# Kernel tuning notes

Measured on AMD Instinct MI355X. Metric: run time of the kernel, lower is better.

## Reference

```python
import jax, jax.numpy as jnp
from jax import lax
import numpy as np

B, C, H, W = 4, 256, 128, 128
NC, NH = 19, 8
HD = C // NH
SCALE = HD ** -0.5
MOM = 0.1

def conv2d(x, w, b=None, pad=0, groups=1):
    y = lax.conv_general_dilated(x, w, (1, 1), [(pad, pad), (pad, pad)],
                                 dimension_numbers=('NCHW', 'OIHW', 'NCHW'),
                                 feature_group_count=groups)
    return y if b is None else y + b[None, :, None, None]

def layernorm(x, g, b, eps=1e-5):
    # LN over channel dim (original permutes to NHWC, LN, permutes back)
    mu = x.mean(1, keepdims=True)
    var = jnp.mean((x - mu) ** 2, 1, keepdims=True)
    return (x - mu) / jnp.sqrt(var + eps) * g[None, :, None, None] + b[None, :, None, None]

def setup_inputs():
    key = jax.random.key(0)
    ks = jax.random.split(key, 24)
    s = 0.02
    mem = jax.random.normal(ks[12], (1, NC, C), jnp.float32)
    mem = mem / jnp.linalg.norm(mem, axis=2, keepdims=True)  # F.normalize(dim=2)
    return dict(
        low=jax.random.normal(ks[0], (B, C, H, W), jnp.float32),
        high=jax.random.normal(ks[1], (B, C, H, W), jnp.float32),
        g_low=jnp.ones((C,), jnp.float32), b_low=jnp.zeros((C,), jnp.float32),
        g_high=jnp.ones((C,), jnp.float32), b_high=jnp.zeros((C,), jnp.float32),
        g_mlp=jnp.ones((C,), jnp.float32), b_mlp=jnp.zeros((C,), jnp.float32),
        w_q_dw=jax.random.normal(ks[2], (C, 1, 3, 3), jnp.float32) * s, b_q_dw=jnp.zeros((C,), jnp.float32),
        w_q_pw=jax.random.normal(ks[3], (C, C, 1, 1), jnp.float32) * s, b_q_pw=jnp.zeros((C,), jnp.float32),
        w_ml1=jax.random.normal(ks[4], (C, C // 4, 1, 1), jnp.float32) * s,
        w_ml2=jax.random.normal(ks[5], (NC, C, 1, 1), jnp.float32) * s,
        w_align=jax.random.normal(ks[6], (C, C // 4, 1, 1), jnp.float32) * s,
        w_kv=jax.random.normal(ks[7], (2 * C, C), jnp.float32) * s, b_kv=jnp.zeros((2 * C,), jnp.float32),
        memory=mem,
        w_proj=jax.random.normal(ks[8], (C, C, 1, 1), jnp.float32) * s, b_proj=jnp.zeros((C,), jnp.float32),
        w_mlp1=jax.random.normal(ks[9], (4 * C, C, 1, 1), jnp.float32) * s, b_mlp1=jnp.zeros((4 * C,), jnp.float32),
        w_mlp_dw=jax.random.normal(ks[10], (4 * C, 1, 3, 3), jnp.float32) * s, b_mlp_dw=jnp.zeros((4 * C,), jnp.float32),
        w_mlp2=jax.random.normal(ks[11], (C, 4 * C, 1, 1), jnp.float32) * s, b_mlp2=jnp.zeros((C,), jnp.float32),
    )

def _cpga(low, high, g_low, b_low, g_high, b_high, g_mlp, b_mlp,
          w_q_dw, b_q_dw, w_q_pw, b_q_pw, w_ml1, w_ml2, w_align,
          w_kv, b_kv, memory, w_proj, b_proj,
          w_mlp1, b_mlp1, w_mlp_dw, b_mlp_dw, w_mlp2, b_mlp2):
    query = layernorm(low, g_low, b_low)
    kv_in = layernorm(high, g_high, b_high)
    fused = (query + kv_in) * 0.5
    # CFEmbedding: learned class mask -> spatial softmax -> class prototypes
    mask = conv2d(conv2d(fused, w_ml1, groups=4), w_ml2)           # [B,NC,H,W]
    mask = jax.nn.softmax(mask.reshape(B, NC, H * W), axis=-1)
    xa = conv2d(fused, w_align, groups=4).reshape(B, C, H * W)
    cf = jnp.einsum('bnl,bcl->bnc', mask, xa)                      # [B,NC,C]
    cf = (1.0 - MOM) * cf + MOM * memory                           # memory mix (eval mode)
    kv = jnp.einsum('bnc,dc->bnd', cf, w_kv) + b_kv                # [B,NC,2C]
    k, v = jnp.split(kv, 2, axis=-1)                               # [B,NC,C] each
    # query path: depthwise-separable 3x3 conv
    q = conv2d(query, w_q_dw, b_q_dw, pad=1, groups=C)
    q = conv2d(q, w_q_pw, b_q_pw).reshape(B, NH, HD, H * W)        # [B,NH,HD,HW]
    kh = k.reshape(B, NC, NH, HD)
    vh = v.reshape(B, NC, NH, HD)
    attn = jnp.einsum('bhdl,bnhd->bhln', q, kh) * SCALE            # [B,NH,HW,NC]
    attn = jnp.max(attn, axis=-1, keepdims=True) - attn            # custom max-subtract
    attn = jax.nn.softmax(attn, axis=-1)
    out = jnp.einsum('bhln,bnhd->bhdl', attn, vh).reshape(B, C, H, W)
    out = conv2d(out, w_proj, b_proj) + low                        # residual 1
    # conv FFN: 1x1 expand -> depthwise 3x3 -> GELU -> 1x1 project
    y = layernorm(out, g_mlp, b_mlp)
    y = conv2d(y, w_mlp1, b_mlp1)
    y = conv2d(y, w_mlp_dw, b_mlp_dw, pad=1, groups=4 * C)
    y = jax.nn.gelu(y, approximate=False)
    y = conv2d(y, w_mlp2, b_mlp2)
    return out + y                                                 # residual 2

def reference(low, high, g_low, b_low, g_high, b_high, g_mlp, b_mlp,
              w_q_dw, b_q_dw, w_q_pw, b_q_pw, w_ml1, w_ml2, w_align,
              w_kv, b_kv, memory, w_proj, b_proj,
              w_mlp1, b_mlp1, w_mlp_dw, b_mlp_dw, w_mlp2, b_mlp2):
    return _cpga(low, high, g_low, b_low, g_high, b_high, g_mlp, b_mlp,
                 w_q_dw, b_q_dw, w_q_pw, b_q_pw, w_ml1, w_ml2, w_align,
                 w_kv, b_kv, memory, w_proj, b_proj,
                 w_mlp1, b_mlp1, w_mlp_dw, b_mlp_dw, w_mlp2, b_mlp2)
```

## Files before the change

kernel.cpp:

```cpp
#include <hip/hip_runtime.h>
#include <hip/hip_bf16.h>
#include <math.h>

using bf16 = __hip_bfloat16;
typedef __attribute__((ext_vector_type(8))) short bf16x8s;
typedef __attribute__((ext_vector_type(4))) float f32x4;

#define HWD 16384
#define CD 256
#define BD 4
#define NCD 19
#define SCALE_F 0.17677669529663687f

#define O_GLOW    0
#define O_BLOW    256
#define O_GHIGH   512
#define O_BHIGH   768
#define O_GMLP    1024
#define O_BMLP    1280
#define O_WQDW    1536
#define O_BQDW    3840
#define O_WQPW    4096
#define O_BQPW    69632
#define O_WML1    69888
#define O_WML2    86272
#define O_WALIGN  91136
#define O_WKV     107520
#define O_BKV     238592
#define O_MEM     239104
#define O_WPROJ   243968
#define O_BPROJ   309504
#define O_WMLP1   309760
#define O_BMLP1   571904
#define O_WMLPDW  572928
#define O_BMLPDW  582144
#define O_WMLP2   583168
#define O_BMLP2   845312
#define WTOTAL    845568

__device__ __forceinline__ float bfv(const bf16* p){ return __bfloat162float(*p); }
__device__ __forceinline__ float ldi(const void* p, size_t i, bool f32){
  return f32 ? ((const float*)p)[i] : __bfloat162float(((const bf16*)p)[i]);
}
__device__ __forceinline__ void sto(void* p, size_t i, float v, bool f32){
  if (f32) ((float*)p)[i] = v; else ((bf16*)p)[i] = __float2bfloat16(v);
}

__device__ __forceinline__ void gld16(const bf16* g, bf16* l){
  __builtin_amdgcn_global_load_lds(
      (const __attribute__((address_space(1))) unsigned int*)g,
      (__attribute__((address_space(3))) unsigned int*)l, 16, 0, 0);
}

__global__ void detect_kernel(const unsigned* __restrict__ g, int* __restrict__ flag){
  if (threadIdx.x == 0) *flag = (g[0] == 0x3F800000u) ? 1 : 0;
}

struct WSrc { const void* p[24]; };
__global__ __launch_bounds__(256) void convert_kernel(WSrc a, bf16* __restrict__ WB,
                                                      const int* __restrict__ flag){
  const bool fin = *flag != 0;
  const int SZ[24] = {256,256,256,256,256,256, 2304,256, 65536,256,
                      16384,4864,16384, 131072,512,4864, 65536,256,
                      262144,1024, 9216,1024, 262144,256};
  size_t i = (size_t)blockIdx.x*256 + threadIdx.x;
  if (i >= WTOTAL) return;
  size_t base = 0; int seg = 0; size_t loc = 0;
  #pragma unroll
  for (int s = 0; s < 24; s++){
    if (i >= base && i < base + (size_t)SZ[s]){ seg = s; loc = i - base; }
    base += (size_t)SZ[s];
  }
  WB[i] = __float2bfloat16(ldi(a.p[seg], loc, fin));
}

__global__ __launch_bounds__(256) void ln_fuse_kernel(
    const void* __restrict__ low, const void* __restrict__ high,
    const bf16* __restrict__ WB, bf16* __restrict__ Q, bf16* __restrict__ F,
    const int* __restrict__ flag){
  const bool fin = *flag != 0;
  union SMU { float red[16][64][4]; bf16 tile[64][256]; };
  __shared__ SMU sm;
  __shared__ float stats[4][64];
  int t = threadIdx.x;
  int pq = t & 15, cs = t >> 4;
  int lg0 = blockIdx.x * 64;
  int b = lg0 >> 14, ll0 = lg0 & (HWD-1);
  size_t pbase = (size_t)b*CD*HWD + (size_t)ll0 + pq*4;
  int c0 = cs*16;

  float s1[4]={0,0,0,0}, s2[4]={0,0,0,0}, u1[4]={0,0,0,0}, u2[4]={0,0,0,0};
  for (int k=0;k<16;k++){
    size_t off = pbase + (size_t)(c0+k)*HWD;
    float xl[4], xh[4];
    if (fin){
      float4 a = *(const float4*)((const float*)low + off);
      float4 h = *(const float4*)((const float*)high + off);
      xl[0]=a.x; xl[1]=a.y; xl[2]=a.z; xl[3]=a.w;
      xh[0]=h.x; xh[1]=h.y; xh[2]=h.z; xh[3]=h.w;
    } else {
      ushort4 a = *(const ushort4*)((const bf16*)low + off);
      ushort4 h = *(const ushort4*)((const bf16*)high + off);
      const bf16* ap=(const bf16*)&a; const bf16* hp=(const bf16*)&h;
      #pragma unroll
      for (int q=0;q<4;q++){ xl[q]=__bfloat162float(ap[q]); xh[q]=__bfloat162float(hp[q]); }
    }
    #pragma unroll
    for (int q=0;q<4;q++){
      s1[q]+=xl[q]; s2[q]+=xl[q]*xl[q];
      u1[q]+=xh[q]; u2[q]+=xh[q]*xh[q];
    }
  }
  #pragma unroll
  for (int q=0;q<4;q++){
    sm.red[cs][pq*4+q][0]=s1[q]; sm.red[cs][pq*4+q][1]=s2[q];
    sm.red[cs][pq*4+q][2]=u1[q]; sm.red[cs][pq*4+q][3]=u2[q];
  }
  __syncthreads();
  if (t < 64){
    float a=0.f,b2=0.f,c=0.f,d=0.f;
    #pragma unroll
    for (int j=0;j<16;j++){
      a+=sm.red[j][t][0]; b2+=sm.red[j][t][1];
      c+=sm.red[j][t][2]; d+=sm.red[j][t][3];
    }
    float ml=a*(1.f/CD), vl=b2*(1.f/CD)-ml*ml;
    float mh=c*(1.f/CD), vh=d*(1.f/CD)-mh*mh;
    stats[0][t]=ml; stats[1][t]=rsqrtf(vl+1e-5f);
    stats[2][t]=mh; stats[3][t]=rsqrtf(vh+1e-5f);
  }
  __syncthreads();
  float mlq[4],rlq[4],mhq[4],rhq[4];
  #pragma unroll
  for (int q=0;q<4;q++){
    mlq[q]=stats[0][pq*4+q]; rlq[q]=stats[1][pq*4+q];
    mhq[q]=stats[2][pq*4+q]; rhq[q]=stats[3][pq*4+q];
  }

  for (int k=0;k<16;k++){
    int c = c0+k;
    size_t off = pbase + (size_t)c*HWD;
    float xl[4];
    if (fin){
      float4 a = *(const float4*)((const float*)low + off);
      xl[0]=a.x; xl[1]=a.y; xl[2]=a.z; xl[3]=a.w;
    } else {
      ushort4 a = *(const ushort4*)((const bf16*)low + off);
      const bf16* ap=(const bf16*)&a;
      #pragma unroll
      for (int q=0;q<4;q++) xl[q]=__bfloat162float(ap[q]);
    }
    float g = bfv(WB+O_GLOW+c), bb = bfv(WB+O_BLOW+c);
    #pragma unroll
    for (int q=0;q<4;q++)
      sm.tile[pq*4+q][c] = __float2bfloat16((xl[q]-mlq[q])*rlq[q]*g + bb);
  }
  __syncthreads();
  {
    bf16* qb = Q + (size_t)lg0*CD;
    const uint4* src = (const uint4*)&sm.tile[0][0];
    #pragma unroll
    for (int it=0; it<8; it++)
      *(uint4*)(qb + ((size_t)it*256 + t)*8) = src[it*256 + t];
  }
  __syncthreads();

  for (int k=0;k<16;k++){
    int c = c0+k;
    size_t off = pbase + (size_t)c*HWD;
    float xl[4], xh[4];
    if (fin){
      float4 a = *(const float4*)((const float*)low + off);
      float4 h = *(const float4*)((const float*)high + off);
      xl[0]=a.x; xl[1]=a.y; xl[2]=a.z; xl[3]=a.w;
      xh[0]=h.x; xh[1]=h.y; xh[2]=h.z; xh[3]=h.w;
    } else {
      ushort4 a = *(const ushort4*)((const bf16*)low + off);
      ushort4 h = *(const ushort4*)((const bf16*)high + off);
      const bf16* ap=(const bf16*)&a; const bf16* hp=(const bf16*)&h;
      #pragma unroll
      for (int q=0;q<4;q++){ xl[q]=__bfloat162float(ap[q]); xh[q]=__bfloat162float(hp[q]); }
    }
    float gl = bfv(WB+O_GLOW+c),  bl = bfv(WB+O_BLOW+c);
    float gh = bfv(WB+O_GHIGH+c), bh = bfv(WB+O_BHIGH+c);
    #pragma unroll
    for (int q=0;q<4;q++){
      float qv = (xl[q]-mlq[q])*rlq[q]*gl + bl;
      float hv = (xh[q]-mhq[q])*rhq[q]*gh + bh;
      sm.tile[pq*4+q][c] = __float2bfloat16(0.5f*(qv+hv));
    }
  }
  __syncthreads();
  {
    bf16* fb = F + (size_t)lg0*CD;
    const uint4* src = (const uint4*)&sm.tile[0][0];
    #pragma unroll
    for (int it=0; it<8; it++)
      *(uint4*)(fb + ((size_t)it*256 + t)*8) = src[it*256 + t];
  }
}

__global__ __launch_bounds__(256) void ln_kernel(
    const bf16* __restrict__ x, const bf16* __restrict__ WB, bf16* __restrict__ out){
  int lg = blockIdx.x*256 + threadIdx.x;
  const bf16* xr = x + (size_t)lg*CD;
  float s1=0.f, s2=0.f;
  for (int v8=0; v8<32; v8++){
    uint4 vv = *(const uint4*)(xr + v8*8);
    const bf16* bb = (const bf16*)&vv;
    #pragma unroll
    for (int i=0;i<8;i++){ float x0 = __bfloat162float(bb[i]); s1+=x0; s2+=x0*x0; }
  }
  float m = s1*(1.f/CD), v = s2*(1.f/CD)-m*m, r = rsqrtf(v+1e-5f);
  bf16* orr = out + (size_t)lg*CD;
  for (int v8=0; v8<32; v8++){
    uint4 vv = *(const uint4*)(xr + v8*8);
    const bf16* bb = (const bf16*)&vv;
    #pragma unroll
    for (int i=0;i<8;i++){
      int c = v8*8+i;
      orr[c] = __float2bfloat16((__bfloat162float(bb[i])-m)*r*bfv(WB+O_GMLP+c) + bfv(WB+O_BMLP+c));
    }
  }
}

template<int K, bool GROUPED, int OUTMODE, int RESMODE, bool HASBIAS, bool SWAP>
__global__ __launch_bounds__(256) void gemm_kernel(
    const bf16* __restrict__ X, int xstride,
    const bf16* __restrict__ W, const bf16* __restrict__ bias,
    const void* __restrict__ resv, void* __restrict__ outv,
    int ostride, int co_limit, int out_off, const int* __restrict__ flag){
  __shared__ bf16 As[64*32];
  __shared__ bf16 Bs[256*32];
  int t = threadIdx.x, w = t>>6, lane = t&63;
  int l0 = blockIdx.x*256;
  int co0 = blockIdx.y*64;
  int koff = GROUPED ? co0 : 0;
  f32x4 acc[4][4];
  #pragma unroll
  for (int i=0;i<4;i++)
    #pragma unroll
    for (int j=0;j<4;j++) acc[i][j] = (f32x4){0.f,0.f,0.f,0.f};

  int sub = lane>>2, kp = lane&3;
  int a_co = co0 + w*16 + sub; if (a_co >= co_limit) a_co = co_limit-1;
  const bf16* aW = W + (size_t)a_co*K + kp*8;
  const bf16* bRow = X + (size_t)(l0 + w*64 + sub)*xstride + koff + kp*8;
  bf16* aL = As + w*512;
  int frow = lane & 15, fk = (lane>>4)*8;
  const bf16* xrd = Bs + ((w*64 + frow)*32 + fk);
  const bf16* wrd = As + (frow*32 + fk);

  for (int k0 = 0; k0 < K; k0 += 32){
    __syncthreads();
    gld16(aW + k0, aL);
    #pragma unroll
    for (int j=0;j<4;j++)
      gld16(bRow + (size_t)j*16*xstride + k0, Bs + (size_t)(w*4+j)*512);
    __syncthreads();
    bf16x8s xf[4], wf[4];
    #pragma unroll
    for (int i=0;i<4;i++){
      xf[i] = *(const bf16x8s*)(xrd + i*512);
      wf[i] = *(const bf16x8s*)(wrd + i*512);
    }
    #pragma unroll
    for (int i=0;i<4;i++)
      #pragma unroll
      for (int j=0;j<4;j++)
        acc[i][j] = SWAP
          ? __builtin_amdgcn_mfma_f32_16x16x32_bf16(wf[i], xf[j], acc[i][j], 0,0,0)
          : __builtin_amdgcn_mfma_f32_16x16x32_bf16(xf[i], wf[j], acc[i][j], 0,0,0);
  }

  const bool fio = *flag != 0;
  #pragma unroll
  for (int i=0;i<4;i++){
    #pragma unroll
    for (int j=0;j<4;j++){
      #pragma unroll
      for (int r=0;r<4;r++){
        int l, co;
        if (SWAP){ co = co0 + i*16 + (lane>>4)*4 + r; l = l0 + w*64 + j*16 + (lane&15); }
        else     { l = l0 + w*64 + i*16 + (lane>>4)*4 + r; co = co0 + j*16 + (lane&15); }
        float v = acc[i][j][r];
        if (HASBIAS) v += __bfloat162float(bias[co]);
        if (RESMODE==2){
          int b = l>>14, ll = l & (HWD-1);
          v += ldi(resv, ((size_t)(b*CD+co))*HWD + ll, fio);
        }
        if (RESMODE==1) v += __bfloat162float(((const bf16*)resv)[(size_t)l*CD + co]);
        if (OUTMODE==0) ((bf16*)outv)[(size_t)l*ostride + co] = __float2bfloat16(v);
        else if (OUTMODE==1){ if (co < co_limit) ((float*)outv)[(size_t)l*ostride + co] = v; }
        else sto(outv, (size_t)out_off + (size_t)co*HWD + l, v, fio);
      }
    }
  }
}

template<int CH, bool GELU>
__global__ __launch_bounds__(256) void dw3x3_kernel(
    const bf16* __restrict__ x, const bf16* __restrict__ w,
    const bf16* __restrict__ bias, bf16* __restrict__ out){
  constexpr int CPG = CH/8;
  constexpr int PPI = 256/CPG;
  constexpr int PPB = PPI*8;
  int t = threadIdx.x;
  int cg = t % CPG, pr = t / CPG;
  int c0 = cg*8;
  float wv[8][9], bv[8];
  #pragma unroll
  for (int i=0;i<8;i++){
    bv[i] = __bfloat162float(bias[c0+i]);
    #pragma unroll
    for (int k=0;k<9;k++) wv[i][k] = __bfloat162float(w[(c0+i)*9+k]);
  }
  int p0 = blockIdx.x * PPB;
  for (int it=0; it<8; it++){
    int px = p0 + it*PPI + pr;
    int l = px & (HWD-1);
    int y = l >> 7, xx = l & 127;
    float acc[8];
    #pragma unroll
    for (int i=0;i<8;i++) acc[i] = bv[i];
    #pragma unroll
    for (int dy=-1;dy<=1;dy++){
      int yy = y+dy; if ((unsigned)yy >= 128u) continue;
      #pragma unroll
      for (int dx=-1;dx<=1;dx++){
        int x2 = xx+dx; if ((unsigned)x2 >= 128u) continue;
        const bf16* pp = x + ((size_t)px + dy*128 + dx)*CH + c0;
        uint4 vv = *(const uint4*)pp;
        const bf16* bb = (const bf16*)&vv;
        #pragma unroll
        for (int i=0;i<8;i++) acc[i] += wv[i][(dy+1)*3+dx+1]*__bfloat162float(bb[i]);
      }
    }
    bf16* orow = out + (size_t)px*CH + c0;
    #pragma unroll
    for (int i=0;i<8;i++){
      float v = acc[i];
      if (GELU) v = 0.5f*v*(1.f+erff(v*0.70710678118f));
      orow[i] = __float2bfloat16(v);
    }
  }
}

__global__ __launch_bounds__(256) void pmax_kernel(const float* __restrict__ M, float* __restrict__ PMX){
  int b = blockIdx.y, tile = blockIdx.x, t = threadIdx.x;
  float mx[NCD];
  #pragma unroll
  for (int n=0;n<NCD;n++) mx[n] = -1e30f;
  for (int p = t; p < 512; p += 256){
    const float* r = M + ((size_t)b*HWD + tile*512 + p)*NCD;
    #pragma unroll
    for (int n=0;n<NCD;n++) mx[n] = fmaxf(mx[n], r[n]);
  }
  int lane = t&63, wv = t>>6;
  __shared__ float red[4][NCD];
  #pragma unroll
  for (int n=0;n<NCD;n++){
    float v = mx[n];
    for (int o=32;o;o>>=1) v = fmaxf(v, __shfl_down(v,o));
    if (lane==0) red[wv][n] = v;
  }
  __syncthreads();
  if (t < NCD)
    PMX[(b*32+tile)*NCD + t] = fmaxf(fmaxf(red[0][t],red[1][t]), fmaxf(red[2][t],red[3][t]));
}

__global__ void fmax_kernel(const float* __restrict__ PMX, float* __restrict__ MX, float* __restrict__ DEN){
  int t = threadIdx.x;
  if (t < BD*NCD){
    int b = t / NCD, n = t % NCD;
    float v = -1e30f;
    for (int i=0;i<32;i++) v = fmaxf(v, PMX[(b*32+i)*NCD + n]);
    MX[t] = v; DEN[t] = 0.f;
  }
}

__global__ __launch_bounds__(256) void exp_kernel(float* __restrict__ M,
    const float* __restrict__ MX, float* __restrict__ DEN){
  int b = blockIdx.y, t = threadIdx.x;
  float* r = M + ((size_t)b*HWD + blockIdx.x*256 + t)*NCD;
  float den[NCD];
  #pragma unroll
  for (int n=0;n<NCD;n++){ float e = expf(r[n] - MX[b*NCD+n]); r[n] = e; den[n] = e; }
  int lane = t&63, wv = t>>6;
  __shared__ float red[4][NCD];
  #pragma unroll
  for (int n=0;n<NCD;n++){
    float v = den[n];
    for (int o=32;o;o>>=1) v += __shfl_down(v,o);
    if (lane==0) red[wv][n] = v;
  }
  __syncthreads();
  if (t < NCD) atomicAdd(&DEN[b*NCD+t], red[0][t]+red[1][t]+red[2][t]+red[3][t]);
}

__global__ __launch_bounds__(256) void cfp_kernel(const float* __restrict__ M,
    const bf16* __restrict__ xa, float* __restrict__ PCF){
  int b = blockIdx.y, lt = blockIdx.x, c = threadIdx.x;
  float acc[NCD];
  #pragma unroll
  for (int n=0;n<NCD;n++) acc[n] = 0.f;
  for (int p=0;p<256;p++){
    size_t l = (size_t)b*HWD + lt*256 + p;
    float xv = __bfloat162float(xa[l*CD + c]);
    const float* e = M + l*NCD;
    #pragma unroll
    for (int n=0;n<NCD;n++) acc[n] += e[n]*xv;
  }
  float* o = PCF + ((size_t)(b*64+lt)*NCD)*CD + c;
  #pragma unroll
  for (int n=0;n<NCD;n++) o[n*CD] = acc[n];
}

__global__ __launch_bounds__(256) void cfr_kernel(const float* __restrict__ PCF,
    const float* __restrict__ DEN, float* __restrict__ CF){
  int idx = blockIdx.x*256 + threadIdx.x;
  if (idx >= BD*NCD*CD) return;
  int c = idx & 255, bn = idx >> 8;
  int b = bn / NCD, n = bn % NCD;
  float s = 0.f;
  for (int lt=0; lt<64; lt++) s += PCF[((size_t)(b*64+lt)*NCD + n)*CD + c];
  CF[(size_t)bn*CD + c] = s / DEN[b*NCD+n];
}

__global__ __launch_bounds__(256) void kv_kernel(const float* __restrict__ CF,
    const bf16* __restrict__ WB, float* __restrict__ KV){
  int idx = blockIdx.x*256 + threadIdx.x;
  if (idx >= BD*NCD*512) return;
  int d = idx & 511, bn = idx >> 9;
  int n = bn % NCD;
  float acc = bfv(WB + O_BKV + d);
  const float* cfr = CF + (size_t)bn*CD;
  const bf16* mr = WB + O_MEM + n*CD;
  const bf16* wr = WB + O_WKV + (size_t)d*CD;
  for (int c=0;c<CD;c++)
    acc += (0.9f*cfr[c] + 0.1f*bfv(mr+c)) * bfv(wr+c);
  KV[(size_t)bn*512 + d] = acc;
}

__global__ __launch_bounds__(256) void attn_kernel(const bf16* __restrict__ q,
    const float* __restrict__ KV, bf16* __restrict__ out){
  __shared__ float ks[NCD][256], vs[NCD][256];
  int t = threadIdx.x;
  int b = blockIdx.y, lt = blockIdx.x;
  for (int i=t; i<NCD*512; i+=256){
    int n = i>>9, d = i&511;
    float v = KV[(size_t)(b*NCD+n)*512 + d];
    if (d < 256) ks[n][d] = v; else vs[n][d-256] = v;
  }
  __syncthreads();
  int p = t & 31, h = t >> 5;
  size_t lg = (size_t)b*HWD + lt*32 + p;
  const bf16* qr = q + lg*CD + h*32;
  float qd[32];
  #pragma unroll
  for (int v8=0; v8<4; v8++){
    uint4 vv = *(const uint4*)(qr + v8*8);
    const bf16* bb = (const bf16*)&vv;
    #pragma unroll
    for (int i=0;i<8;i++) qd[v8*8+i] = __bfloat162float(bb[i]);
  }
  float s[NCD];
  #pragma unroll
  for (int n=0;n<NCD;n++){
    const float* kr = &ks[n][h*32];
    float a = 0.f;
    #pragma unroll
    for (int d=0;d<32;d++) a += qd[d]*kr[d];
    s[n] = a * SCALE_F;
  }
  float mn = s[0];
  #pragma unroll
  for (int n=1;n<NCD;n++) mn = fminf(mn, s[n]);
  float sum = 0.f;
  #pragma unroll
  for (int n=0;n<NCD;n++){ s[n] = expf(mn - s[n]); sum += s[n]; }
  float inv = 1.f/sum;
  bf16* orow = out + lg*CD + h*32;
  #pragma unroll
  for (int d=0;d<32;d++){
    float o = 0.f;
    #pragma unroll
    for (int n=0;n<NCD;n++) o += s[n]*vs[n][h*32+d];
    orow[d] = __float2bfloat16(o*inv);
  }
}

extern "C" void kernel_launch(void* const* d_in, const int* in_sizes, int n_in,
                              void* d_out, int out_size, void* d_ws, size_t ws_size,
                              hipStream_t stream){
  const void* low  = d_in[0];
  const void* high = d_in[1];

  char* ws = (char*)d_ws;
  bf16* B1 = (bf16*)(ws);
  bf16* B2 = (bf16*)(ws + ((size_t)32<<20));
  bf16* B3 = (bf16*)(ws + ((size_t)64<<20));
  bf16* B4 = (bf16*)(ws + ((size_t)96<<20));
  float* M  = (float*)(ws + ((size_t)128<<20));
  float* PCF= (float*)(ws + ((size_t)134<<20));
  bf16* WB  = (bf16*)(ws + ((size_t)140<<20));
  float* PMX= (float*)(ws + ((size_t)142<<20));
  float* MX = (float*)(ws + ((size_t)142<<20) + (64<<10));
  float* DEN= (float*)(ws + ((size_t)142<<20) + (80<<10));
  float* CF = (float*)(ws + ((size_t)142<<20) + (96<<10));
  float* KV = (float*)(ws + ((size_t)142<<20) + (256<<10));
  int* FLAG = (int*)  (ws + ((size_t)142<<20) + (512<<10));

  dim3 blk(256);

  detect_kernel<<<1, 64, 0, stream>>>((const unsigned*)d_in[2], FLAG);

  WSrc src;
  for (int i=0;i<24;i++) src.p[i] = d_in[i+2];
  convert_kernel<<<(WTOTAL+255)/256, blk, 0, stream>>>(src, WB, FLAG);

  ln_fuse_kernel<<<1024, blk, 0, stream>>>(low, high, WB, B1, B2, FLAG);
  gemm_kernel<64,true,0,0,false,false><<<dim3(256,4), blk, 0, stream>>>(
      B2, 256, WB+O_WML1, nullptr, nullptr, B3, 256, 256, 0, FLAG);
  gemm_kernel<256,false,1,0,false,false><<<dim3(256,1), blk, 0, stream>>>(
      B3, 256, WB+O_WML2, nullptr, nullptr, M, NCD, NCD, 0, FLAG);
  pmax_kernel<<<dim3(32,BD), blk, 0, stream>>>(M, PMX);
  fmax_kernel<<<1, 128, 0, stream>>>(PMX, MX, DEN);
  exp_kernel<<<dim3(64,BD), blk, 0, stream>>>(M, MX, DEN);
  gemm_kernel<64,true,0,0,false,false><<<dim3(256,4), blk, 0, stream>>>(
      B2, 256, WB+O_WALIGN, nullptr, nullptr, B3, 256, 256, 0, FLAG);
  cfp_kernel<<<dim3(64,BD), blk, 0, stream>>>(M, B3, PCF);
  cfr_kernel<<<(BD*NCD*CD+255)/256, blk, 0, stream>>>(PCF, DEN, CF);
  kv_kernel<<<(BD*NCD*512+255)/256, blk, 0, stream>>>(CF, WB, KV);
  dw3x3_kernel<256,false><<<1024, blk, 0, stream>>>(B1, WB+O_WQDW, WB+O_BQDW, B2);
  gemm_kernel<256,false,0,0,true,false><<<dim3(256,4), blk, 0, stream>>>(
      B2, 256, WB+O_WQPW, WB+O_BQPW, nullptr, B3, 256, 256, 0, FLAG);
  attn_kernel<<<dim3(512,BD), blk, 0, stream>>>(B3, KV, B2);
  gemm_kernel<256,false,0,2,true,false><<<dim3(256,4), blk, 0, stream>>>(
      B2, 256, WB+O_WPROJ, WB+O_BPROJ, low, B1, 256, 256, 0, FLAG);
  ln_kernel<<<256, blk, 0, stream>>>(B1, WB, B2);
  for (int b = 0; b < BD; b++){
    gemm_kernel<256,false,0,0,true,false><<<dim3(64,16), blk, 0, stream>>>(
        B2 + (size_t)b*HWD*CD, 256, WB+O_WMLP1, WB+O_BMLP1, nullptr, B3, 1024, 1024, 0, FLAG);
    dw3x3_kernel<1024,true><<<1024, blk, 0, stream>>>(B3, WB+O_WMLPDW, WB+O_BMLPDW, B4);
    gemm_kernel<1024,false,2,1,true,true><<<dim3(64,4), blk, 0, stream>>>(
        B4, 1024, WB+O_WMLP2, WB+O_BMLP2, B1 + (size_t)b*HWD*CD, d_out, 0, 256, b*CD*HWD, FLAG);
  }
}
```

Measured before the change: 945.7 us.

## Swizzle LN shared tile, fuse global passes, add smaller L-tile GEMM variants

The LN fuse kernel now reads low/high only once in its final pass. It keeps the averaged values in registers while writing the normalized low tile to shared memory with an XOR swizzle, which avoids bank conflicts on the column-strided stores. It also gets a launch-bounds occupancy hint. The GEMM kernel gains an L-tile template parameter, so the 19-class GEMM and the K=1024 MLP2 projection run with 128-row tiles and twice as many blocks, improving occupancy on under-filled launches. The trade-offs are more register pressure from the 64-float register array and less weight reuse per block.

```diff
diff --git a/kernel.cpp b/kernel.cpp
--- a/kernel.cpp
+++ b/kernel.cpp
@@ -74,7 +74,9 @@
   WB[i] = __float2bfloat16(ldi(a.p[seg], loc, fin));
 }
 
-__global__ __launch_bounds__(256) void ln_fuse_kernel(
+#define TSWZ(row, c) ((c) ^ (((row) >> 2) << 3))
+
+__global__ __launch_bounds__(256, 4) void ln_fuse_kernel(
     const void* __restrict__ low, const void* __restrict__ high,
     const bf16* __restrict__ WB, bf16* __restrict__ Q, bf16* __restrict__ F,
     const int* __restrict__ flag){
@@ -137,34 +139,8 @@
     mhq[q]=stats[2][pq*4+q]; rhq[q]=stats[3][pq*4+q];
   }
 
-  for (int k=0;k<16;k++){
-    int c = c0+k;
-    size_t off = pbase + (size_t)c*HWD;
-    float xl[4];
-    if (fin){
-      float4 a = *(const float4*)((const float*)low + off);
-      xl[0]=a.x; xl[1]=a.y; xl[2]=a.z; xl[3]=a.w;
-    } else {
-      ushort4 a = *(const ushort4*)((const bf16*)low + off);
-      const bf16* ap=(const bf16*)&a;
-      #pragma unroll
-      for (int q=0;q<4;q++) xl[q]=__bfloat162float(ap[q]);
-    }
-    float g = bfv(WB+O_GLOW+c), bb = bfv(WB+O_BLOW+c);
-    #pragma unroll
-    for (int q=0;q<4;q++)
-      sm.tile[pq*4+q][c] = __float2bfloat16((xl[q]-mlq[q])*rlq[q]*g + bb);
-  }
-  __syncthreads();
-  {
-    bf16* qb = Q + (size_t)lg0*CD;
-    const uint4* src = (const uint4*)&sm.tile[0][0];
-    #pragma unroll
-    for (int it=0; it<8; it++)
-      *(uint4*)(qb + ((size_t)it*256 + t)*8) = src[it*256 + t];
-  }
-  __syncthreads();
-
+  float fv[16][4];
+  #pragma unroll
   for (int k=0;k<16;k++){
     int c = c0+k;
     size_t off = pbase + (size_t)c*HWD;
@@ -185,18 +161,42 @@
     float gh = bfv(WB+O_GHIGH+c), bh = bfv(WB+O_BHIGH+c);
     #pragma unroll
     for (int q=0;q<4;q++){
+      int row = pq*4+q;
       float qv = (xl[q]-mlq[q])*rlq[q]*gl + bl;
       float hv = (xh[q]-mhq[q])*rhq[q]*gh + bh;
-      sm.tile[pq*4+q][c] = __float2bfloat16(0.5f*(qv+hv));
+      sm.tile[row][TSWZ(row, c)] = __float2bfloat16(qv);
+      fv[k][q] = 0.5f*(qv+hv);
+    }
+  }
+  __syncthreads();
+  {
+    bf16* qb = Q + (size_t)lg0*CD;
+    #pragma unroll
+    for (int it=0; it<8; it++){
+      int idx = it*256 + t;
+      int row = idx >> 5, col = (idx & 31)*8;
+      *(uint4*)(qb + (size_t)idx*8) = *(const uint4*)(&sm.tile[row][TSWZ(row, col)]);
+    }
+  }
+  __syncthreads();
+  #pragma unroll
+  for (int k=0;k<16;k++){
+    int c = c0+k;
+    #pragma unroll
+    for (int q=0;q<4;q++){
+      int row = pq*4+q;
+      sm.tile[row][TSWZ(row, c)] = __float2bfloat16(fv[k][q]);
     }
   }
   __syncthreads();
   {
     bf16* fb = F + (size_t)lg0*CD;
-    const uint4* src = (const uint4*)&sm.tile[0][0];
-    #pragma unroll
-    for (int it=0; it<8; it++)
-      *(uint4*)(fb + ((size_t)it*256 + t)*8) = src[it*256 + t];
+    #pragma unroll
+    for (int it=0; it<8; it++){
+      int idx = it*256 + t;
+      int row = idx >> 5, col = (idx & 31)*8;
+      *(uint4*)(fb + (size_t)idx*8) = *(const uint4*)(&sm.tile[row][TSWZ(row, col)]);
+    }
   }
 }
 
@@ -224,16 +224,19 @@
   }
 }
 
-template<int K, bool GROUPED, int OUTMODE, int RESMODE, bool HASBIAS, bool SWAP>
+template<int LT, int K, bool GROUPED, int OUTMODE, int RESMODE, bool HASBIAS, bool SWAP>
 __global__ __launch_bounds__(256) void gemm_kernel(
     const bf16* __restrict__ X, int xstride,
     const bf16* __restrict__ W, const bf16* __restrict__ bias,
     const void* __restrict__ resv, void* __restrict__ outv,
     int ostride, int co_limit, int out_off, const int* __restrict__ flag){
+  constexpr int IF = LT/64;
+  constexpr int NI = SWAP ? 4 : IF;
+  constexpr int NJ = SWAP ? IF : 4;
   __shared__ bf16 As[64*32];
-  __shared__ bf16 Bs[256*32];
+  __shared__ bf16 Bs[LT*32];
   int t = threadIdx.x, w = t>>6, lane = t&63;
-  int l0 = blockIdx.x*256;
+  int l0 = blockIdx.x*LT;
   int co0 = blockIdx.y*64;
   int koff = GROUPED ? co0 : 0;
   f32x4 acc[4][4];
@@ -245,29 +248,28 @@
   int sub = lane>>2, kp = lane&3;
   int a_co = co0 + w*16 + sub; if (a_co >= co_limit) a_co = co_limit-1;
   const bf16* aW = W + (size_t)a_co*K + kp*8;
-  const bf16* bRow = X + (size_t)(l0 + w*64 + sub)*xstride + koff + kp*8;
+  const bf16* bRow = X + (size_t)(l0 + w*(LT/4) + sub)*xstride + koff + kp*8;
   bf16* aL = As + w*512;
   int frow = lane & 15, fk = (lane>>4)*8;
-  const bf16* xrd = Bs + ((w*64 + frow)*32 + fk);
+  const bf16* xrd = Bs + ((w*(LT/4) + frow)*32 + fk);
   const bf16* wrd = As + (frow*32 + fk);
 
   for (int k0 = 0; k0 < K; k0 += 32){
     __syncthreads();
     gld16(aW + k0, aL);
     #pragma unroll
-    for (int j=0;j<4;j++)
-      gld16(bRow + (size_t)j*16*xstride + k0, Bs + (size_t)(w*4+j)*512);
+    for (int j=0;j<IF;j++)
+      gld16(bRow + (size_t)j*16*xstride + k0, Bs + (size_t)(w*IF+j)*512);
     __syncthreads();
-    bf16x8s xf[4], wf[4];
-    #pragma unroll
-    for (int i=0;i<4;i++){
-      xf[i] = *(const bf16x8s*)(xrd + i*512);
-      wf[i] = *(const bf16x8s*)(wrd + i*512);
-    }
-    #pragma unroll
-    for (int i=0;i<4;i++)
+    bf16x8s xf[IF], wf[4];
+    #pragma unroll
+    for (int i=0;i<IF;i++) xf[i] = *(const bf16x8s*)(xrd + i*512);
+    #pragma unroll
+    for (int i=0;i<4;i++)  wf[i] = *(const bf16x8s*)(wrd + i*512);
+    #pragma unroll
+    for (int i=0;i<NI;i++)
       #pragma unroll
-      for (int j=0;j<4;j++)
+      for (int j=0;j<NJ;j++)
         acc[i][j] = SWAP
           ? __builtin_amdgcn_mfma_f32_16x16x32_bf16(wf[i], xf[j], acc[i][j], 0,0,0)
           : __builtin_amdgcn_mfma_f32_16x16x32_bf16(xf[i], wf[j], acc[i][j], 0,0,0);
@@ -275,14 +277,14 @@
 
   const bool fio = *flag != 0;
   #pragma unroll
-  for (int i=0;i<4;i++){
-    #pragma unroll
-    for (int j=0;j<4;j++){
+  for (int i=0;i<NI;i++){
+    #pragma unroll
+    for (int j=0;j<NJ;j++){
       #pragma unroll
       for (int r=0;r<4;r++){
         int l, co;
-        if (SWAP){ co = co0 + i*16 + (lane>>4)*4 + r; l = l0 + w*64 + j*16 + (lane&15); }
-        else     { l = l0 + w*64 + i*16 + (lane>>4)*4 + r; co = co0 + j*16 + (lane&15); }
+        if (SWAP){ co = co0 + i*16 + (lane>>4)*4 + r; l = l0 + w*(LT/4) + j*16 + (lane&15); }
+        else     { l = l0 + w*(LT/4) + i*16 + (lane>>4)*4 + r; co = co0 + j*16 + (lane&15); }
         float v = acc[i][j][r];
         if (HASBIAS) v += __bfloat162float(bias[co]);
         if (RESMODE==2){
@@ -520,30 +522,30 @@
   convert_kernel<<<(WTOTAL+255)/256, blk, 0, stream>>>(src, WB, FLAG);
 
   ln_fuse_kernel<<<1024, blk, 0, stream>>>(low, high, WB, B1, B2, FLAG);
-  gemm_kernel<64,true,0,0,false,false><<<dim3(256,4), blk, 0, stream>>>(
+  gemm_kernel<256,64,true,0,0,false,false><<<dim3(256,4), blk, 0, stream>>>(
       B2, 256, WB+O_WML1, nullptr, nullptr, B3, 256, 256, 0, FLAG);
-  gemm_kernel<256,false,1,0,false,false><<<dim3(256,1), blk, 0, stream>>>(
+  gemm_kernel<128,256,false,1,0,false,false><<<dim3(512,1), blk, 0, stream>>>(
       B3, 256, WB+O_WML2, nullptr, nullptr, M, NCD, NCD, 0, FLAG);
   pmax_kernel<<<dim3(32,BD), blk, 0, stream>>>(M, PMX);
   fmax_kernel<<<1, 128, 0, stream>>>(PMX, MX, DEN);
   exp_kernel<<<dim3(64,BD), blk, 0, stream>>>(M, MX, DEN);
-  gemm_kernel<64,true,0,0,false,false><<<dim3(256,4), blk, 0, stream>>>(
+  gemm_kernel<256,64,true,0,0,false,false><<<dim3(256,4), blk, 0, stream>>>(
       B2, 256, WB+O_WALIGN, nullptr, nullptr, B3, 256, 256, 0, FLAG);
   cfp_kernel<<<dim3(64,BD), blk, 0, stream>>>(M, B3, PCF);
   cfr_kernel<<<(BD*NCD*CD+255)/256, blk, 0, stream>>>(PCF, DEN, CF);
   kv_kernel<<<(BD*NCD*512+255)/256, blk, 0, stream>>>(CF, WB, KV);
   dw3x3_kernel<256,false><<<1024, blk, 0, stream>>>(B1, WB+O_WQDW, WB+O_BQDW, B2);
-  gemm_kernel<256,false,0,0,true,false><<<dim3(256,4), blk, 0, stream>>>(
+  gemm_kernel<256,256,false,0,0,true,false><<<dim3(256,4), blk, 0, stream>>>(
       B2, 256, WB+O_WQPW, WB+O_BQPW, nullptr, B3, 256, 256, 0, FLAG);
   attn_kernel<<<dim3(512,BD), blk, 0, stream>>>(B3, KV, B2);
-  gemm_kernel<256,false,0,2,true,false><<<dim3(256,4), blk, 0, stream>>>(
+  gemm_kernel<256,256,false,0,2,true,false><<<dim3(256,4), blk, 0, stream>>>(
       B2, 256, WB+O_WPROJ, WB+O_BPROJ, low, B1, 256, 256, 0, FLAG);
   ln_kernel<<<256, blk, 0, stream>>>(B1, WB, B2);
   for (int b = 0; b < BD; b++){
-    gemm_kernel<256,false,0,0,true,false><<<dim3(64,16), blk, 0, stream>>>(
+    gemm_kernel<256,256,false,0,0,true,false><<<dim3(64,16), blk, 0, stream>>>(
         B2 + (size_t)b*HWD*CD, 256, WB+O_WMLP1, WB+O_BMLP1, nullptr, B3, 1024, 1024, 0, FLAG);
     dw3x3_kernel<1024,true><<<1024, blk, 0, stream>>>(B3, WB+O_WMLPDW, WB+O_BMLPDW, B4);
-    gemm_kernel<1024,false,2,1,true,true><<<dim3(64,4), blk, 0, stream>>>(
+    gemm_kernel<128,1024,false,2,1,true,true><<<dim3(128,4), blk, 0, stream>>>(
         B4, 1024, WB+O_WMLP2, WB+O_BMLP2, B1 + (size_t)b*HWD*CD, d_out, 0, 256, b*CD*HWD, FLAG);
   }
 }
```

Result: no change. 962.0 us (+1.7%).
